# Optimization experiments

Measured on AMD Instinct MI355X. Metric: run time of the kernel, lower is better.

## Reference

```python
import jax, jax.numpy as jnp
import numpy as np

NUM_HEADS = 16
NUM_KV_HEADS = 4
HEAD_DIM = 64
HIDDEN = 1024
R_SOFTPLUS_0 = 1.442695041


def setup_inputs() -> dict:
    key = jax.random.key(0)
    ks = jax.random.split(key, 6)
    B, S = 2, 2048
    qkv_out = (NUM_HEADS + 2 * NUM_KV_HEADS) * HEAD_DIM  # 1536
    return {
        "hidden_states": jax.random.normal(ks[0], (B, S, HIDDEN), dtype=jnp.float32),
        "scaling": jax.random.normal(ks[1], (HEAD_DIM,), dtype=jnp.float32),
        "qkv_w": jax.random.normal(ks[2], (qkv_out, HIDDEN), dtype=jnp.float32) * (1.0 / np.sqrt(HIDDEN)),
        "qkv_b": jax.random.normal(ks[3], (qkv_out,), dtype=jnp.float32) * 0.01,
        "o_w": jax.random.normal(ks[4], (HIDDEN, NUM_HEADS * HEAD_DIM), dtype=jnp.float32) * (1.0 / np.sqrt(NUM_HEADS * HEAD_DIM)),
        "o_b": jax.random.normal(ks[5], (HIDDEN,), dtype=jnp.float32) * 0.01,
    }


def reference(hidden_states, scaling, qkv_w, qkv_b, o_w, o_b):
    B, S, _ = hidden_states.shape
    H, KV, D = NUM_HEADS, NUM_KV_HEADS, HEAD_DIM
    rep = H // KV

    qkv = hidden_states @ qkv_w.T + qkv_b  # [B,S,(H+2KV)*D]
    xq, xk, xv = jnp.split(qkv, [H * D, H * D + KV * D], axis=-1)
    xq = xq.reshape(B, S, H, D)
    xk = xk.reshape(B, S, KV, D)
    xv = xv.reshape(B, S, KV, D)

    # per-dim softplus scaling of queries
    scale = (R_SOFTPLUS_0 / jnp.sqrt(jnp.float32(D))) * jax.nn.softplus(scaling)
    xq = xq * scale[None, None, None, :]

    # GQA: repeat kv heads to match query heads
    xk = jnp.repeat(xk, rep, axis=2)  # [B,S,H,D]
    xv = jnp.repeat(xv, rep, axis=2)

    scores = jnp.einsum("bqhd,bkhd->bhqk", xq, xk)  # [B,H,S,S]
    probs = jax.nn.softmax(scores.astype(jnp.float32), axis=-1).astype(xq.dtype)
    out = jnp.einsum("bhqk,bkhd->bqhd", probs, xv)  # [B,S,H,D]
    out = out.reshape(B, S, H * D)
    return out @ o_w.T + o_b
```

## Files before the change

### kernel.cpp

```cpp
#include <hip/hip_runtime.h>
#include <stdint.h>

#define HQ 16
#define HKV 4
#define DH 64
#define HID 1024
#define QKVN 1536
#define SEQ 2048
#define NB 2
#define NTOK 4096

typedef __bf16 bf16x8 __attribute__((ext_vector_type(8)));
typedef __bf16 bf16x2 __attribute__((ext_vector_type(2)));
typedef float f32x4 __attribute__((ext_vector_type(4)));
typedef float f32x16 __attribute__((ext_vector_type(16)));
typedef unsigned int u32;
typedef unsigned short u16;

__device__ __forceinline__ u32 pk(float lo, float hi) {
  bf16x2 t;
  t[0] = (__bf16)lo;
  t[1] = (__bf16)hi;
  return __builtin_bit_cast(u32, t);
}
__device__ __forceinline__ u16 bf1(float f) {
  return __builtin_bit_cast(u16, (__bf16)f);
}

__device__ __forceinline__ void gl_lds16(const void* g, void* l) {
  __builtin_amdgcn_global_load_lds(
      (__attribute__((address_space(1))) u32*)(uintptr_t)g,
      (__attribute__((address_space(3))) u32*)(u32)(uintptr_t)l, 16, 0, 0);
}

#if __has_builtin(__builtin_amdgcn_exp2f)
#define EXP2(x) __builtin_amdgcn_exp2f(x)
#else
#define EXP2(x) __expf((x) * 0.69314718055994531f)
#endif

#if __has_builtin(__builtin_amdgcn_fdot2_f32_bf16)
#define HAVE_DOT2 1
#endif

#define FENCE() asm volatile("" ::: "memory")

__global__ void cvt_bf16_kernel(const float* __restrict__ h,
                                const float* __restrict__ w1,
                                const float* __restrict__ w2,
                                u16* __restrict__ oh, u16* __restrict__ ow1,
                                u16* __restrict__ ow2) {
  const int NH = NTOK * HID / 8, NW1 = QKVN * HID / 8, NW2 = HID * HID / 8;
  int idx = blockIdx.x * blockDim.x + threadIdx.x;
  if (idx >= NH + NW1 + NW2) return;
  const float* s; u16* d; int o;
  if (idx < NH) { s = h; d = oh; o = idx; }
  else if (idx < NH + NW1) { s = w1; d = ow1; o = idx - NH; }
  else { s = w2; d = ow2; o = idx - NH - NW1; }
  const float4* sp = (const float4*)s + (size_t)o * 2;
  float4 a = sp[0], b = sp[1];
  uint4 out;
  out.x = pk(a.x, a.y);
  out.y = pk(a.z, a.w);
  out.z = pk(b.x, b.y);
  out.w = pk(b.z, b.w);
  *((uint4*)(d + (size_t)o * 8)) = out;
}

template <int EPI>
__global__ __launch_bounds__(256, 3) void gemm_nt_kernel(
    const u16* __restrict__ A, const u16* __restrict__ Bw,
    const float* __restrict__ bias, const float* __restrict__ scaling,
    void* __restrict__ Out, int ldout) {
  constexpr int BM = 64;
  constexpr int MR = BM / 32;
  constexpr int ACH = BM / 32;
  constexpr int BUF = BM * 128 + 16384;
  __shared__ char smem[2 * BUF];
  const int tid = threadIdx.x;
  const int lane = tid & 63, wid = tid >> 6;
  const int l15 = lane & 15, lg = lane >> 4;
  const int wr = wid >> 1, wc = wid & 1;
  const int mt = blockIdx.x * BM, nt = blockIdx.y * 128;

  const u16* ag[ACH]; const u16* bg[4]; int al[ACH]; int bl[4];
#pragma unroll
  for (int c = 0; c < ACH; c++) {
    int chunk = wid * ACH + c;
    int rp = chunk * 8 + (lane >> 3);
    int lb = (lane & 7) ^ (rp & 7);
    ag[c] = A + (size_t)(mt + rp) * HID + lb * 8;
    al[c] = chunk * 1024;
  }
#pragma unroll
  for (int c = 0; c < 4; c++) {
    int chunk = wid * 4 + c;
    int rp = chunk * 8 + (lane >> 3);
    int lb = (lane & 7) ^ (rp & 7);
    bg[c] = Bw + (size_t)(nt + rp) * HID + lb * 8;
    bl[c] = BM * 128 + chunk * 1024;
  }

  f32x4 acc[MR][4] = {};

#pragma unroll
  for (int c = 0; c < ACH; c++) gl_lds16(ag[c], smem + al[c]);
#pragma unroll
  for (int c = 0; c < 4; c++) gl_lds16(bg[c], smem + bl[c]);

  for (int kt = 0; kt < HID / 64; kt++) {
    const int cur = (kt & 1) * BUF;
    const int nxt = BUF - cur;
    if (kt < HID / 64 - 1) {
#pragma unroll
      for (int c = 0; c < ACH; c++) gl_lds16(ag[c] + (kt + 1) * 64, smem + nxt + al[c]);
#pragma unroll
      for (int c = 0; c < 4; c++) gl_lds16(bg[c] + (kt + 1) * 64, smem + nxt + bl[c]);
      asm volatile("s_waitcnt vmcnt(6)" ::: "memory");
    } else {
      asm volatile("s_waitcnt vmcnt(0)" ::: "memory");
    }
    __builtin_amdgcn_s_barrier();
    FENCE();
    const char* Asm = smem + cur;
    const char* Bsm = smem + cur + BM * 128;
#pragma unroll
    for (int kk = 0; kk < 2; kk++) {
      bf16x8 af[MR], bfr[4];
#pragma unroll
      for (int mi = 0; mi < MR; mi++) {
        int row = wr * (BM / 2) + mi * 16 + l15;
        int blk = kk * 4 + lg;
        af[mi] = *(const bf16x8*)(Asm + row * 128 + ((blk ^ (row & 7)) << 4));
      }
#pragma unroll
      for (int nj = 0; nj < 4; nj++) {
        int row = wc * 64 + nj * 16 + l15;
        int blk = kk * 4 + lg;
        bfr[nj] = *(const bf16x8*)(Bsm + row * 128 + ((blk ^ (row & 7)) << 4));
      }
#pragma unroll
      for (int mi = 0; mi < MR; mi++)
#pragma unroll
        for (int nj = 0; nj < 4; nj++)
          acc[mi][nj] = __builtin_amdgcn_mfma_f32_16x16x32_bf16(af[mi], bfr[nj],
                                                                acc[mi][nj], 0, 0, 0);
    }
    FENCE();
    __builtin_amdgcn_s_barrier();
    FENCE();
  }

  if (EPI == 0) {
    float qs[4];
#pragma unroll
    for (int nj = 0; nj < 4; nj++) {
      int col = nt + wc * 64 + nj * 16 + l15;
      if (col < HQ * DH) {
        float x = scaling[col & 63];
        float sp = (x > 15.f) ? x : log1pf(__expf(x));
        qs[nj] = (1.442695041f / 8.0f) * sp * 1.442695041f;
      } else {
        qs[nj] = 1.0f;
      }
    }
    u16* O = (u16*)Out;
#pragma unroll
    for (int mi = 0; mi < MR; mi++)
#pragma unroll
      for (int nj = 0; nj < 4; nj++)
#pragma unroll
        for (int r = 0; r < 4; r++) {
          int row = mt + wr * (BM / 2) + mi * 16 + lg * 4 + r;
          int col = nt + wc * 64 + nj * 16 + l15;
          float v = (acc[mi][nj][r] + bias[col]) * qs[nj];
          O[(size_t)row * ldout + col] = bf1(v);
        }
  } else {
    float* O = (float*)Out;
#pragma unroll
    for (int mi = 0; mi < MR; mi++)
#pragma unroll
      for (int nj = 0; nj < 4; nj++)
#pragma unroll
        for (int r = 0; r < 4; r++) {
          int row = mt + wr * (BM / 2) + mi * 16 + lg * 4 + r;
          int col = nt + wc * 64 + nj * 16 + l15;
          O[(size_t)row * ldout + col] = acc[mi][nj][r] + bias[col];
        }
  }
}

__global__ __launch_bounds__(256) void vtrans_kernel(const u16* __restrict__ qkv,
                                                     u16* __restrict__ vt) {
  __shared__ u16 tile[64][68];
  int tt = blockIdx.x;
  int g = blockIdx.y;
  int b = g >> 2, kv = g & 3;
  int ts = tt * 64;
  int t = threadIdx.x;
#pragma unroll
  for (int pass = 0; pass < 4; pass++) {
    int tok = pass * 16 + (t >> 4);
    int d0 = (t & 15) * 4;
    const u16* src = qkv + (size_t)(b * SEQ + ts + tok) * QKVN + (HQ * DH + HKV * DH) + kv * DH + d0;
    *(uint2*)&tile[tok][d0] = *(const uint2*)src;
  }
  __syncthreads();
#pragma unroll
  for (int pass = 0; pass < 16; pass++) {
    int flat = pass * 256 + t;
    int d = flat >> 6, tok = flat & 63;
    vt[(size_t)(g * 64 + d) * SEQ + ts + tok] = tile[tok][d];
  }
}

__global__ __launch_bounds__(512, 2) void attn_kernel(const u16* __restrict__ qkv,
                                                      const u16* __restrict__ vt,
                                                      u16* __restrict__ aout) {
  __shared__ char smem[65536];
  const int tid = threadIdx.x, lane = tid & 63, wid = tid >> 6;
  const int l31 = lane & 31, hi = lane >> 5;
  const int g = wid >> 2, wg = wid & 3;
  const int kvb = g * 1024;
  const int qt = blockIdx.x, bh = blockIdx.y;
  const int b = bh >> 4, h = bh & 15, kvh = h >> 2;
  const int tb = b * SEQ;

  bf16x8 qb[2][4];
#pragma unroll
  for (int qc = 0; qc < 2; qc++)
#pragma unroll
    for (int kk = 0; kk < 4; kk++) {
      int row = tb + qt * 256 + wg * 64 + qc * 32 + l31;
      qb[qc][kk] = *(const bf16x8*)(qkv + (size_t)row * QKVN + h * DH + kk * 16 + hi * 8);
    }

  const int rsub = lane >> 3;
  const int gsw = ((lane & 7) ^ rsub) * 8;
  const u16* kgb[2]; const u16* vgb[2]; int klo[2], vlo[2];
#pragma unroll
  for (int c = 0; c < 2; c++) {
    int ch = wg * 2 + c;
    int rp = ch * 8 + rsub;
    int ktok = (rp & ~12) | ((rp & 4) << 1) | ((rp & 8) >> 1);
    kgb[c] = qkv + (size_t)(tb + kvb + ktok) * QKVN + HQ * DH + kvh * DH + gsw;
    vgb[c] = vt + (size_t)((b * HKV + kvh) * DH + rp) * SEQ + kvb + gsw;
    klo[c] = g * 16384 + ch * 1024;
    vlo[c] = g * 16384 + 8192 + ch * 1024;
  }

  f32x16 ot[2][2] = {};
  float l_run[2] = {0.f, 0.f};

#pragma unroll
  for (int c = 0; c < 2; c++) {
    gl_lds16(kgb[c], smem + klo[c]);
    gl_lds16(vgb[c], smem + vlo[c]);
    kgb[c] += 64 * QKVN;
    vgb[c] += 64;
  }

  const int swz = l31 & 7;

  for (int kt = 0; kt < 16; kt++) {
    const int cur = (kt & 1) * 32768;
    const int nxt = 32768 - cur;
    if (kt < 15) {
#pragma unroll
      for (int c = 0; c < 2; c++) {
        gl_lds16(kgb[c], smem + nxt + klo[c]);
        gl_lds16(vgb[c], smem + nxt + vlo[c]);
        kgb[c] += 64 * QKVN;
        vgb[c] += 64;
      }
      asm volatile("s_waitcnt vmcnt(4)" ::: "memory");
    } else {
      asm volatile("s_waitcnt vmcnt(0)" ::: "memory");
    }
    __builtin_amdgcn_s_barrier();
    FENCE();

    const char* Ks = smem + cur + g * 16384;
    const char* Vs = Ks + 8192;

    f32x16 s[2][2] = {};
#pragma unroll
    for (int kk = 0; kk < 4; kk++) {
      int gp = kk * 2 + hi;
      bf16x8 ka0 = *(const bf16x8*)(Ks + l31 * 128 + ((gp ^ swz) << 4));
      bf16x8 ka1 = *(const bf16x8*)(Ks + (l31 + 32) * 128 + ((gp ^ swz) << 4));
#pragma unroll
      for (int qc = 0; qc < 2; qc++) {
        s[qc][0] = __builtin_amdgcn_mfma_f32_32x32x16_bf16(ka0, qb[qc][kk], s[qc][0], 0, 0, 0);
        s[qc][1] = __builtin_amdgcn_mfma_f32_32x32x16_bf16(ka1, qb[qc][kk], s[qc][1], 0, 0, 0);
      }
    }

#pragma unroll
    for (int qc = 0; qc < 2; qc++)
#pragma unroll
      for (int hf = 0; hf < 2; hf++)
#pragma unroll
        for (int i = 0; i < 16; i++) s[qc][hf][i] = EXP2(s[qc][hf][i]);

    float lsum[2] = {0.f, 0.f};
#ifdef HAVE_DOT2
    const bf16x2 ones2 = {(__bf16)1.0f, (__bf16)1.0f};
#endif
#ifndef HAVE_DOT2
#pragma unroll
    for (int qc = 0; qc < 2; qc++) {
      float ts[16];
#pragma unroll
      for (int i = 0; i < 16; i++) ts[i] = s[qc][0][i] + s[qc][1][i];
#pragma unroll
      for (int st = 8; st > 0; st >>= 1)
#pragma unroll
        for (int i = 0; i < 8; i++)
          if (i < st) ts[i] += ts[i + st];
      lsum[qc] = ts[0];
    }
#endif
#pragma unroll
    for (int ck = 0; ck < 4; ck++) {
      int gp = ck * 2 + hi;
      bf16x8 va0 = *(const bf16x8*)(Vs + l31 * 128 + ((gp ^ swz) << 4));
      bf16x8 va1 = *(const bf16x8*)(Vs + (l31 + 32) * 128 + ((gp ^ swz) << 4));
#pragma unroll
      for (int qc = 0; qc < 2; qc++) {
        const int hf = (ck < 2) ? 0 : 1;
        const int base = (ck & 1) * 8;
        union { u32 u[4]; bf16x8 v; } pu;
        pu.u[0] = pk(s[qc][hf][base + 0], s[qc][hf][base + 1]);
        pu.u[1] = pk(s[qc][hf][base + 2], s[qc][hf][base + 3]);
        pu.u[2] = pk(s[qc][hf][base + 4], s[qc][hf][base + 5]);
        pu.u[3] = pk(s[qc][hf][base + 6], s[qc][hf][base + 7]);
#ifdef HAVE_DOT2
#pragma unroll
        for (int w = 0; w < 4; w++)
          lsum[qc] = __builtin_amdgcn_fdot2_f32_bf16(
              __builtin_bit_cast(bf16x2, pu.u[w]), ones2, lsum[qc], false);
#endif
        ot[qc][0] = __builtin_amdgcn_mfma_f32_32x32x16_bf16(va0, pu.v, ot[qc][0], 0, 0, 0);
        ot[qc][1] = __builtin_amdgcn_mfma_f32_32x32x16_bf16(va1, pu.v, ot[qc][1], 0, 0, 0);
      }
    }
#pragma unroll
    for (int qc = 0; qc < 2; qc++)
      l_run[qc] += lsum[qc] + __shfl_xor(lsum[qc], 32);
    FENCE();
    __builtin_amdgcn_s_barrier();
    FENCE();
  }

  float* exf = (float*)smem;
  __syncthreads();
  if (wid >= 4) {
    int idx = tid - 256;
#pragma unroll
    for (int j = 0; j < 16; j++) exf[j * 256 + idx] = ot[0][0][j];
#pragma unroll
    for (int j = 0; j < 16; j++) exf[(16 + j) * 256 + idx] = ot[0][1][j];
    ((float*)(smem + 32768))[idx] = l_run[0];
    ((float*)(smem + 33792))[idx] = l_run[1];
  }
  __syncthreads();
  if (wid < 4) {
#pragma unroll
    for (int j = 0; j < 16; j++) ot[0][0][j] += exf[j * 256 + tid];
#pragma unroll
    for (int j = 0; j < 16; j++) ot[0][1][j] += exf[(16 + j) * 256 + tid];
    l_run[0] += ((const float*)(smem + 32768))[tid];
    l_run[1] += ((const float*)(smem + 33792))[tid];
  }
  __syncthreads();
  if (wid >= 4) {
    int idx = tid - 256;
#pragma unroll
    for (int j = 0; j < 16; j++) exf[j * 256 + idx] = ot[1][0][j];
#pragma unroll
    for (int j = 0; j < 16; j++) exf[(16 + j) * 256 + idx] = ot[1][1][j];
  }
  __syncthreads();
  if (wid < 4) {
#pragma unroll
    for (int j = 0; j < 16; j++) ot[1][0][j] += exf[j * 256 + tid];
#pragma unroll
    for (int j = 0; j < 16; j++) ot[1][1][j] += exf[(16 + j) * 256 + tid];
  }
  __syncthreads();

  u16* Ot = (u16*)smem;
  if (wid < 4) {
#pragma unroll
    for (int qc = 0; qc < 2; qc++) {
      float inv = 1.0f / l_run[qc];
      const int qrow_l = wg * 64 + qc * 32 + l31;
#pragma unroll
      for (int hf = 0; hf < 2; hf++)
#pragma unroll
        for (int rq = 0; rq < 4; rq++) {
          int d0 = hf * 32 + rq * 8 + 4 * hi;
          float v0 = ot[qc][hf][rq * 4 + 0], v1 = ot[qc][hf][rq * 4 + 1];
          float v2 = ot[qc][hf][rq * 4 + 2], v3 = ot[qc][hf][rq * 4 + 3];
          u32 wa = pk(v0 * inv, v1 * inv);
          u32 wb = pk(v2 * inv, v3 * inv);
          int ga = ((d0 >> 3) ^ (qrow_l & 7));
          *(u32*)((char*)Ot + qrow_l * 128 + ga * 16 + ((d0 & 7) << 1)) = wa;
          *(u32*)((char*)Ot + qrow_l * 128 + ga * 16 + (((d0 + 2) & 7) << 1)) = wb;
        }
    }
  }
  __syncthreads();
#pragma unroll
  for (int it = 0; it < 4; it++) {
    int gidx = it * 512 + tid;
    int row = gidx >> 3, c8 = gidx & 7;
    int pos = c8 ^ (row & 7);
    uint4 val = *(const uint4*)((const char*)Ot + row * 128 + pos * 16);
    *(uint4*)(aout + (size_t)(tb + qt * 256 + row) * (HQ * DH) + h * DH + c8 * 8) = val;
  }
}

extern "C" void kernel_launch(void* const* d_in, const int* in_sizes, int n_in,
                              void* d_out, int out_size, void* d_ws, size_t ws_size,
                              hipStream_t stream) {
  const float* hs = (const float*)d_in[0];
  const float* scaling = (const float*)d_in[1];
  const float* qkv_w = (const float*)d_in[2];
  const float* qkv_b = (const float*)d_in[3];
  const float* o_w = (const float*)d_in[4];
  const float* o_b = (const float*)d_in[5];
  float* out = (float*)d_out;

  char* ws = (char*)d_ws;
  u16* h_bf = (u16*)ws;
  u16* w1_bf = (u16*)(ws + 8388608);
  u16* w2_bf = (u16*)(ws + 11534336);
  u16* qkv = (u16*)(ws + 13631488);
  u16* vtb = (u16*)(ws + 26214400);
  u16* att = (u16*)(ws + 28311552);

  {
    int tot = (NTOK * HID + QKVN * HID + HID * HID) / 8;
    cvt_bf16_kernel<<<(tot + 255) / 256, 256, 0, stream>>>(hs, qkv_w, o_w, h_bf, w1_bf, w2_bf);
  }
  gemm_nt_kernel<0><<<dim3(NTOK / 64, QKVN / 128), 256, 0, stream>>>(
      h_bf, w1_bf, qkv_b, scaling, qkv, QKVN);
  vtrans_kernel<<<dim3(SEQ / 64, NB * HKV), 256, 0, stream>>>(qkv, vtb);
  attn_kernel<<<dim3(SEQ / 256, NB * HQ), 512, 0, stream>>>(qkv, vtb, att);
  gemm_nt_kernel<1><<<dim3(NTOK / 64, HID / 128), 256, 0, stream>>>(
      att, w2_bf, o_b, nullptr, out, HID);
}
```

Measured before the change: 81.23 us.

## Fuse V transpose into QKV GEMM epilogue and split attention KV four ways

Removes the separate V-transpose kernel. The QKV GEMM epilogue now also writes the V columns transposed into the vt buffer, with scattered 2-byte stores. The attention kernel's query tile shrinks from 256 to 128 rows, so the grid is twice as large. Its 8 waves now split the KV sequence four ways (512 tokens each) with 2 query waves per group, with a new V LDS layout and a two-stage cross-wave reduction. This aims to improve occupancy and SM fill and cut one launch, at the cost of more reduction work and uncoalesced transposed stores in the GEMM.

```diff
diff --git a/kernel.cpp b/kernel.cpp
--- a/kernel.cpp
+++ b/kernel.cpp
@@ -71,7 +71,7 @@
 __global__ __launch_bounds__(256, 3) void gemm_nt_kernel(
     const u16* __restrict__ A, const u16* __restrict__ Bw,
     const float* __restrict__ bias, const float* __restrict__ scaling,
-    void* __restrict__ Out, int ldout) {
+    void* __restrict__ Out, int ldout, u16* __restrict__ vt) {
   constexpr int BM = 64;
   constexpr int MR = BM / 32;
   constexpr int ACH = BM / 32;
@@ -176,6 +176,22 @@
           float v = (acc[mi][nj][r] + bias[col]) * qs[nj];
           O[(size_t)row * ldout + col] = bf1(v);
         }
+    if (nt >= (HQ + HKV) * DH) {
+#pragma unroll
+      for (int mi = 0; mi < MR; mi++)
+#pragma unroll
+        for (int nj = 0; nj < 4; nj++)
+#pragma unroll
+          for (int r = 0; r < 4; r++) {
+            int row = mt + wr * (BM / 2) + mi * 16 + lg * 4 + r;
+            int col = nt + wc * 64 + nj * 16 + l15;
+            int vc = col - (HQ + HKV) * DH;
+            int kv = vc >> 6, d = vc & 63;
+            int b = row >> 11, tok = row & (SEQ - 1);
+            float v = acc[mi][nj][r] + bias[col];
+            vt[((size_t)(b * HKV + kv) * DH + d) * SEQ + tok] = bf1(v);
+          }
+    }
   } else {
     float* O = (float*)Out;
 #pragma unroll
@@ -191,38 +207,14 @@
   }
 }
 
-__global__ __launch_bounds__(256) void vtrans_kernel(const u16* __restrict__ qkv,
-                                                     u16* __restrict__ vt) {
-  __shared__ u16 tile[64][68];
-  int tt = blockIdx.x;
-  int g = blockIdx.y;
-  int b = g >> 2, kv = g & 3;
-  int ts = tt * 64;
-  int t = threadIdx.x;
-#pragma unroll
-  for (int pass = 0; pass < 4; pass++) {
-    int tok = pass * 16 + (t >> 4);
-    int d0 = (t & 15) * 4;
-    const u16* src = qkv + (size_t)(b * SEQ + ts + tok) * QKVN + (HQ * DH + HKV * DH) + kv * DH + d0;
-    *(uint2*)&tile[tok][d0] = *(const uint2*)src;
-  }
-  __syncthreads();
-#pragma unroll
-  for (int pass = 0; pass < 16; pass++) {
-    int flat = pass * 256 + t;
-    int d = flat >> 6, tok = flat & 63;
-    vt[(size_t)(g * 64 + d) * SEQ + ts + tok] = tile[tok][d];
-  }
-}
-
-__global__ __launch_bounds__(512, 2) void attn_kernel(const u16* __restrict__ qkv,
-                                                      const u16* __restrict__ vt,
+__global__ __launch_bounds__(512, 4) void attn_kernel(const u16* __restrict__ qkv,
+                                                      const u16* __restrict__ vtb,
                                                       u16* __restrict__ aout) {
   __shared__ char smem[65536];
   const int tid = threadIdx.x, lane = tid & 63, wid = tid >> 6;
   const int l31 = lane & 31, hi = lane >> 5;
-  const int g = wid >> 2, wg = wid & 3;
-  const int kvb = g * 1024;
+  const int g = wid >> 1, wq = wid & 1;
+  const int kvb = g * 512;
   const int qt = blockIdx.x, bh = blockIdx.y;
   const int b = bh >> 4, h = bh & 15, kvh = h >> 2;
   const int tb = b * SEQ;
@@ -232,36 +224,43 @@
   for (int qc = 0; qc < 2; qc++)
 #pragma unroll
     for (int kk = 0; kk < 4; kk++) {
-      int row = tb + qt * 256 + wg * 64 + qc * 32 + l31;
+      int row = tb + qt * 128 + wq * 64 + qc * 32 + l31;
       qb[qc][kk] = *(const bf16x8*)(qkv + (size_t)row * QKVN + h * DH + kk * 16 + hi * 8);
     }
 
-  const int rsub = lane >> 3;
-  const int gsw = ((lane & 7) ^ rsub) * 8;
-  const u16* kgb[2]; const u16* vgb[2]; int klo[2], vlo[2];
+  const u16* kg[2]; const u16* vg[2]; int klo[2], vlo[2];
 #pragma unroll
   for (int c = 0; c < 2; c++) {
-    int ch = wg * 2 + c;
-    int rp = ch * 8 + rsub;
-    int ktok = (rp & ~12) | ((rp & 4) << 1) | ((rp & 8) >> 1);
-    kgb[c] = qkv + (size_t)(tb + kvb + ktok) * QKVN + HQ * DH + kvh * DH + gsw;
-    vgb[c] = vt + (size_t)((b * HKV + kvh) * DH + rp) * SEQ + kvb + gsw;
-    klo[c] = g * 16384 + ch * 1024;
-    vlo[c] = g * 16384 + 8192 + ch * 1024;
-  }
-
-  f32x16 ot[2][2] = {};
-  float l_run[2] = {0.f, 0.f};
+    int ch = wq * 2 + c;
+    {
+      int slot = ch * 64 + lane;
+      int krow = slot >> 3, ks = slot & 7;
+      int kd = (ks ^ (krow & 7)) * 8;
+      int ktok = (krow & ~12) | ((krow & 4) << 1) | ((krow & 8) >> 1);
+      kg[c] = qkv + (size_t)(tb + kvb + ktok) * QKVN + HQ * DH + kvh * DH + kd;
+      klo[c] = g * 8192 + ch * 1024;
+    }
+    {
+      int slot = ch * 64 + lane;
+      int vR = slot >> 3, vs = slot & 7;
+      int vp = vs ^ (vR & 7);
+      int vd = 2 * vR + (vp >> 2);
+      int vgb = vp & 3;
+      vg[c] = vtb + (size_t)((b * HKV + kvh) * DH + vd) * SEQ + kvb + vgb * 8;
+      vlo[c] = g * 8192 + 4096 + ch * 1024;
+    }
+  }
+
+  f32x16 ot00 = {}, ot01 = {}, ot10 = {}, ot11 = {};
+  float l0 = 0.f, l1 = 0.f;
 
 #pragma unroll
   for (int c = 0; c < 2; c++) {
-    gl_lds16(kgb[c], smem + klo[c]);
-    gl_lds16(vgb[c], smem + vlo[c]);
-    kgb[c] += 64 * QKVN;
-    vgb[c] += 64;
-  }
-
-  const int swz = l31 & 7;
+    gl_lds16(kg[c], smem + klo[c]);
+    gl_lds16(vg[c], smem + vlo[c]);
+    kg[c] += 32 * QKVN;
+    vg[c] += 32;
+  }
 
   for (int kt = 0; kt < 16; kt++) {
     const int cur = (kt & 1) * 32768;
@@ -269,10 +268,10 @@
     if (kt < 15) {
 #pragma unroll
       for (int c = 0; c < 2; c++) {
-        gl_lds16(kgb[c], smem + nxt + klo[c]);
-        gl_lds16(vgb[c], smem + nxt + vlo[c]);
-        kgb[c] += 64 * QKVN;
-        vgb[c] += 64;
+        gl_lds16(kg[c], smem + nxt + klo[c]);
+        gl_lds16(vg[c], smem + nxt + vlo[c]);
+        kg[c] += 32 * QKVN;
+        vg[c] += 32;
       }
       asm volatile("s_waitcnt vmcnt(4)" ::: "memory");
     } else {
@@ -281,129 +280,147 @@
     __builtin_amdgcn_s_barrier();
     FENCE();
 
-    const char* Ks = smem + cur + g * 16384;
-    const char* Vs = Ks + 8192;
-
-    f32x16 s[2][2] = {};
+    const char* Ks = smem + cur + g * 8192;
+    const char* Vs = Ks + 4096;
+
+    f32x16 sa = {}, sb = {};
 #pragma unroll
     for (int kk = 0; kk < 4; kk++) {
-      int gp = kk * 2 + hi;
-      bf16x8 ka0 = *(const bf16x8*)(Ks + l31 * 128 + ((gp ^ swz) << 4));
-      bf16x8 ka1 = *(const bf16x8*)(Ks + (l31 + 32) * 128 + ((gp ^ swz) << 4));
-#pragma unroll
-      for (int qc = 0; qc < 2; qc++) {
-        s[qc][0] = __builtin_amdgcn_mfma_f32_32x32x16_bf16(ka0, qb[qc][kk], s[qc][0], 0, 0, 0);
-        s[qc][1] = __builtin_amdgcn_mfma_f32_32x32x16_bf16(ka1, qb[qc][kk], s[qc][1], 0, 0, 0);
-      }
-    }
-
-#pragma unroll
-    for (int qc = 0; qc < 2; qc++)
-#pragma unroll
-      for (int hf = 0; hf < 2; hf++)
-#pragma unroll
-        for (int i = 0; i < 16; i++) s[qc][hf][i] = EXP2(s[qc][hf][i]);
-
-    float lsum[2] = {0.f, 0.f};
+      bf16x8 ka = *(const bf16x8*)(Ks + l31 * 128 + (((kk * 2 + hi) ^ (l31 & 7)) << 4));
+      sa = __builtin_amdgcn_mfma_f32_32x32x16_bf16(ka, qb[0][kk], sa, 0, 0, 0);
+      sb = __builtin_amdgcn_mfma_f32_32x32x16_bf16(ka, qb[1][kk], sb, 0, 0, 0);
+    }
+
+#pragma unroll
+    for (int i = 0; i < 16; i++) sa[i] = EXP2(sa[i]);
+#pragma unroll
+    for (int i = 0; i < 16; i++) sb[i] = EXP2(sb[i]);
+
+    float ls0 = 0.f, ls1 = 0.f;
 #ifdef HAVE_DOT2
     const bf16x2 ones2 = {(__bf16)1.0f, (__bf16)1.0f};
+#else
+    {
+#pragma unroll
+      for (int i = 0; i < 16; i++) ls0 += sa[i];
+#pragma unroll
+      for (int i = 0; i < 16; i++) ls1 += sb[i];
+    }
 #endif
-#ifndef HAVE_DOT2
+#pragma unroll
+    for (int kb = 0; kb < 2; kb++) {
+      const int vsw = ((l31 & 1) * 4 + kb * 2 + hi) ^ ((l31 >> 1) & 7);
+      bf16x8 va0 = *(const bf16x8*)(Vs + (l31 >> 1) * 128 + (vsw << 4));
+      bf16x8 va1 = *(const bf16x8*)(Vs + (16 + (l31 >> 1)) * 128 + (vsw << 4));
+      union { u32 u[4]; bf16x8 v; } pa, pb;
+#pragma unroll
+      for (int w = 0; w < 4; w++) {
+        pa.u[w] = pk(sa[kb * 8 + 2 * w], sa[kb * 8 + 2 * w + 1]);
+        pb.u[w] = pk(sb[kb * 8 + 2 * w], sb[kb * 8 + 2 * w + 1]);
+      }
+#ifdef HAVE_DOT2
+#pragma unroll
+      for (int w = 0; w < 4; w++) {
+        ls0 = __builtin_amdgcn_fdot2_f32_bf16(__builtin_bit_cast(bf16x2, pa.u[w]), ones2, ls0, false);
+        ls1 = __builtin_amdgcn_fdot2_f32_bf16(__builtin_bit_cast(bf16x2, pb.u[w]), ones2, ls1, false);
+      }
+#endif
+      ot00 = __builtin_amdgcn_mfma_f32_32x32x16_bf16(va0, pa.v, ot00, 0, 0, 0);
+      ot01 = __builtin_amdgcn_mfma_f32_32x32x16_bf16(va1, pa.v, ot01, 0, 0, 0);
+      ot10 = __builtin_amdgcn_mfma_f32_32x32x16_bf16(va0, pb.v, ot10, 0, 0, 0);
+      ot11 = __builtin_amdgcn_mfma_f32_32x32x16_bf16(va1, pb.v, ot11, 0, 0, 0);
+    }
+    l0 += ls0 + __shfl_xor(ls0, 32);
+    l1 += ls1 + __shfl_xor(ls1, 32);
+    FENCE();
+    __builtin_amdgcn_s_barrier();
+    FENCE();
+  }
+
+  float* ex = (float*)smem;
+  float* exl = (float*)(smem + 32768);
+  const int widx = (wid & 1) | ((wid & 4) >> 1);
+  __syncthreads();
+  if (wid & 2) {
+#pragma unroll
+    for (int j = 0; j < 16; j++) ex[widx * 2048 + j * 64 + lane] = ot00[j];
+#pragma unroll
+    for (int j = 0; j < 16; j++) ex[widx * 2048 + (16 + j) * 64 + lane] = ot01[j];
+    exl[widx * 64 + lane] = l0;
+  }
+  __syncthreads();
+  if (!(wid & 2)) {
+#pragma unroll
+    for (int j = 0; j < 16; j++) ot00[j] += ex[widx * 2048 + j * 64 + lane];
+#pragma unroll
+    for (int j = 0; j < 16; j++) ot01[j] += ex[widx * 2048 + (16 + j) * 64 + lane];
+    l0 += exl[widx * 64 + lane];
+  }
+  __syncthreads();
+  if (wid & 2) {
+#pragma unroll
+    for (int j = 0; j < 16; j++) ex[widx * 2048 + j * 64 + lane] = ot10[j];
+#pragma unroll
+    for (int j = 0; j < 16; j++) ex[widx * 2048 + (16 + j) * 64 + lane] = ot11[j];
+    exl[widx * 64 + lane] = l1;
+  }
+  __syncthreads();
+  if (!(wid & 2)) {
+#pragma unroll
+    for (int j = 0; j < 16; j++) ot10[j] += ex[widx * 2048 + j * 64 + lane];
+#pragma unroll
+    for (int j = 0; j < 16; j++) ot11[j] += ex[widx * 2048 + (16 + j) * 64 + lane];
+    l1 += exl[widx * 64 + lane];
+  }
+  __syncthreads();
+  if ((wid & 6) == 4) {
+    int w2 = wid & 1;
+#pragma unroll
+    for (int j = 0; j < 16; j++) ex[w2 * 4096 + j * 64 + lane] = ot00[j];
+#pragma unroll
+    for (int j = 0; j < 16; j++) ex[w2 * 4096 + (16 + j) * 64 + lane] = ot01[j];
+#pragma unroll
+    for (int j = 0; j < 16; j++) ex[w2 * 4096 + (32 + j) * 64 + lane] = ot10[j];
+#pragma unroll
+    for (int j = 0; j < 16; j++) ex[w2 * 4096 + (48 + j) * 64 + lane] = ot11[j];
+    exl[w2 * 128 + lane * 2 + 0] = l0;
+    exl[w2 * 128 + lane * 2 + 1] = l1;
+  }
+  __syncthreads();
+  if (wid < 2) {
+    int w2 = wid & 1;
+#pragma unroll
+    for (int j = 0; j < 16; j++) ot00[j] += ex[w2 * 4096 + j * 64 + lane];
+#pragma unroll
+    for (int j = 0; j < 16; j++) ot01[j] += ex[w2 * 4096 + (16 + j) * 64 + lane];
+#pragma unroll
+    for (int j = 0; j < 16; j++) ot10[j] += ex[w2 * 4096 + (32 + j) * 64 + lane];
+#pragma unroll
+    for (int j = 0; j < 16; j++) ot11[j] += ex[w2 * 4096 + (48 + j) * 64 + lane];
+    l0 += exl[w2 * 128 + lane * 2 + 0];
+    l1 += exl[w2 * 128 + lane * 2 + 1];
+  }
+  __syncthreads();
+
+  u16* Ot = (u16*)smem;
+  if (wid < 2) {
 #pragma unroll
     for (int qc = 0; qc < 2; qc++) {
-      float ts[16];
-#pragma unroll
-      for (int i = 0; i < 16; i++) ts[i] = s[qc][0][i] + s[qc][1][i];
-#pragma unroll
-      for (int st = 8; st > 0; st >>= 1)
-#pragma unroll
-        for (int i = 0; i < 8; i++)
-          if (i < st) ts[i] += ts[i + st];
-      lsum[qc] = ts[0];
-    }
-#endif
-#pragma unroll
-    for (int ck = 0; ck < 4; ck++) {
-      int gp = ck * 2 + hi;
-      bf16x8 va0 = *(const bf16x8*)(Vs + l31 * 128 + ((gp ^ swz) << 4));
-      bf16x8 va1 = *(const bf16x8*)(Vs + (l31 + 32) * 128 + ((gp ^ swz) << 4));
-#pragma unroll
-      for (int qc = 0; qc < 2; qc++) {
-        const int hf = (ck < 2) ? 0 : 1;
-        const int base = (ck & 1) * 8;
-        union { u32 u[4]; bf16x8 v; } pu;
-        pu.u[0] = pk(s[qc][hf][base + 0], s[qc][hf][base + 1]);
-        pu.u[1] = pk(s[qc][hf][base + 2], s[qc][hf][base + 3]);
-        pu.u[2] = pk(s[qc][hf][base + 4], s[qc][hf][base + 5]);
-        pu.u[3] = pk(s[qc][hf][base + 6], s[qc][hf][base + 7]);
-#ifdef HAVE_DOT2
-#pragma unroll
-        for (int w = 0; w < 4; w++)
-          lsum[qc] = __builtin_amdgcn_fdot2_f32_bf16(
-              __builtin_bit_cast(bf16x2, pu.u[w]), ones2, lsum[qc], false);
-#endif
-        ot[qc][0] = __builtin_amdgcn_mfma_f32_32x32x16_bf16(va0, pu.v, ot[qc][0], 0, 0, 0);
-        ot[qc][1] = __builtin_amdgcn_mfma_f32_32x32x16_bf16(va1, pu.v, ot[qc][1], 0, 0, 0);
-      }
-    }
-#pragma unroll
-    for (int qc = 0; qc < 2; qc++)
-      l_run[qc] += lsum[qc] + __shfl_xor(lsum[qc], 32);
-    FENCE();
-    __builtin_amdgcn_s_barrier();
-    FENCE();
-  }
-
-  float* exf = (float*)smem;
-  __syncthreads();
-  if (wid >= 4) {
-    int idx = tid - 256;
-#pragma unroll
-    for (int j = 0; j < 16; j++) exf[j * 256 + idx] = ot[0][0][j];
-#pragma unroll
-    for (int j = 0; j < 16; j++) exf[(16 + j) * 256 + idx] = ot[0][1][j];
-    ((float*)(smem + 32768))[idx] = l_run[0];
-    ((float*)(smem + 33792))[idx] = l_run[1];
-  }
-  __syncthreads();
-  if (wid < 4) {
-#pragma unroll
-    for (int j = 0; j < 16; j++) ot[0][0][j] += exf[j * 256 + tid];
-#pragma unroll
-    for (int j = 0; j < 16; j++) ot[0][1][j] += exf[(16 + j) * 256 + tid];
-    l_run[0] += ((const float*)(smem + 32768))[tid];
-    l_run[1] += ((const float*)(smem + 33792))[tid];
-  }
-  __syncthreads();
-  if (wid >= 4) {
-    int idx = tid - 256;
-#pragma unroll
-    for (int j = 0; j < 16; j++) exf[j * 256 + idx] = ot[1][0][j];
-#pragma unroll
-    for (int j = 0; j < 16; j++) exf[(16 + j) * 256 + idx] = ot[1][1][j];
-  }
-  __syncthreads();
-  if (wid < 4) {
-#pragma unroll
-    for (int j = 0; j < 16; j++) ot[1][0][j] += exf[j * 256 + tid];
-#pragma unroll
-    for (int j = 0; j < 16; j++) ot[1][1][j] += exf[(16 + j) * 256 + tid];
-  }
-  __syncthreads();
-
-  u16* Ot = (u16*)smem;
-  if (wid < 4) {
-#pragma unroll
-    for (int qc = 0; qc < 2; qc++) {
-      float inv = 1.0f / l_run[qc];
-      const int qrow_l = wg * 64 + qc * 32 + l31;
-#pragma unroll
-      for (int hf = 0; hf < 2; hf++)
+      float inv = 1.0f / (qc == 0 ? l0 : l1);
+      const int qrow_l = wid * 64 + qc * 32 + l31;
+#pragma unroll
+      for (int db = 0; db < 2; db++)
 #pragma unroll
         for (int rq = 0; rq < 4; rq++) {
-          int d0 = hf * 32 + rq * 8 + 4 * hi;
-          float v0 = ot[qc][hf][rq * 4 + 0], v1 = ot[qc][hf][rq * 4 + 1];
-          float v2 = ot[qc][hf][rq * 4 + 2], v3 = ot[qc][hf][rq * 4 + 3];
+          int d0 = db * 32 + rq * 8 + 4 * hi;
+          float v0, v1, v2, v3;
+          if (qc == 0) {
+            const f32x16& o = db ? ot01 : ot00;
+            v0 = o[rq * 4 + 0]; v1 = o[rq * 4 + 1]; v2 = o[rq * 4 + 2]; v3 = o[rq * 4 + 3];
+          } else {
+            const f32x16& o = db ? ot11 : ot10;
+            v0 = o[rq * 4 + 0]; v1 = o[rq * 4 + 1]; v2 = o[rq * 4 + 2]; v3 = o[rq * 4 + 3];
+          }
           u32 wa = pk(v0 * inv, v1 * inv);
           u32 wb = pk(v2 * inv, v3 * inv);
           int ga = ((d0 >> 3) ^ (qrow_l & 7));
@@ -414,12 +431,12 @@
   }
   __syncthreads();
 #pragma unroll
-  for (int it = 0; it < 4; it++) {
+  for (int it = 0; it < 2; it++) {
     int gidx = it * 512 + tid;
     int row = gidx >> 3, c8 = gidx & 7;
     int pos = c8 ^ (row & 7);
     uint4 val = *(const uint4*)((const char*)Ot + row * 128 + pos * 16);
-    *(uint4*)(aout + (size_t)(tb + qt * 256 + row) * (HQ * DH) + h * DH + c8 * 8) = val;
+    *(uint4*)(aout + (size_t)(tb + qt * 128 + row) * (HQ * DH) + h * DH + c8 * 8) = val;
   }
 }
 
@@ -447,9 +464,8 @@
     cvt_bf16_kernel<<<(tot + 255) / 256, 256, 0, stream>>>(hs, qkv_w, o_w, h_bf, w1_bf, w2_bf);
   }
   gemm_nt_kernel<0><<<dim3(NTOK / 64, QKVN / 128), 256, 0, stream>>>(
-      h_bf, w1_bf, qkv_b, scaling, qkv, QKVN);
-  vtrans_kernel<<<dim3(SEQ / 64, NB * HKV), 256, 0, stream>>>(qkv, vtb);
-  attn_kernel<<<dim3(SEQ / 256, NB * HQ), 512, 0, stream>>>(qkv, vtb, att);
+      h_bf, w1_bf, qkv_b, scaling, qkv, QKVN, vtb);
+  attn_kernel<<<dim3(SEQ / 128, NB * HQ), 512, 0, stream>>>(qkv, vtb, att);
   gemm_nt_kernel<1><<<dim3(NTOK / 64, HID / 128), 256, 0, stream>>>(
-      att, w2_bf, o_b, nullptr, out, HID);
-}
+      att, w2_bf, o_b, nullptr, out, HID, nullptr);
+}
```

New measurement: 171.2 us. +110.8%, slower.
